# Optimization experiments

Hardware: AMD Instinct MI355X
Metric: run time of the kernel (lower is better)

Reference implementation:

```python
import jax, jax.numpy as jnp
import numpy as np

HIDDEN = 2048
REDUCTION = 4
DOWN = HIDDEN // REDUCTION  # 512
E = 16
K = 2
B, S = 4, 2048


def setup_inputs() -> dict:
    key = jax.random.key(0)
    k1, k2, k3, k4 = jax.random.split(key, 4)
    x = jax.random.normal(k1, (B, S, HIDDEN), dtype=jnp.float32)
    gate_w = jax.random.normal(k2, (E, HIDDEN), dtype=jnp.float32) * 0.02
    # xavier_uniform over (E, DOWN, HIDDEN): bound = sqrt(6/(DOWN+HIDDEN))
    bound = float(np.sqrt(6.0 / (DOWN + HIDDEN)))
    down_w = jax.random.uniform(k3, (E, DOWN, HIDDEN), dtype=jnp.float32,
                                minval=-bound, maxval=bound)
    down_b = jnp.zeros((E, DOWN), dtype=jnp.float32)
    ub = float(np.sqrt(1.0 / DOWN))
    up_w = jax.random.uniform(k4, (HIDDEN, DOWN), dtype=jnp.float32,
                              minval=-ub, maxval=ub)
    up_b = jnp.zeros((HIDDEN,), dtype=jnp.float32)
    return {"x": x, "gate_w": gate_w, "down_w": down_w, "down_b": down_b,
            "up_w": up_w, "up_b": up_b}


def reference(x, gate_w, down_w, down_b, up_w, up_b):
    Bb, Ss, D = x.shape
    N = Bb * Ss
    xf = x.reshape(N, D)
    # TopKGate: logits -> top-k -> softmax over the k logits -> scatter to full [N,E]
    logits = xf @ gate_w.T                       # [N, E]
    topv, topi = jax.lax.top_k(logits, K)        # [N, K]
    probs = jax.nn.softmax(topv, axis=-1)        # [N, K]
    gw = jnp.zeros_like(logits).at[jnp.arange(N)[:, None], topi].set(probs)  # [N, E]
    # Dense-equivalent of gather + per-token bmm + scatter-add combine:
    # final[n] = sum_e gw[n,e] * (down_w[e] @ x[n] + down_b[e])
    expert_out = jnp.einsum('nd,eod->neo', xf, down_w) + down_b[None]  # [N, E, DOWN]
    combined = jnp.einsum('ne,neo->no', gw, expert_out)                # [N, DOWN]
    h = jax.nn.gelu(combined, approximate=True)  # gelu_new (tanh approx)
    h = h.reshape(Bb, Ss, DOWN)
    out = h @ up_w.T + up_b                      # [B, S, HIDDEN]
    # load balancing loss: E * sum(sum(gw,0)/N * mean(gw,0)) * alpha
    loss = E * jnp.sum(jnp.sum(gw, axis=0) / N * jnp.mean(gw, axis=0)) * 0.1
    return out, loss
```

## Files before the change

kernel.cpp:

```cpp
#include <hip/hip_runtime.h>
#include <hip/hip_bf16.h>
#include <math.h>

#define NTOK   8192
#define HID    2048
#define DWN    512
#define NEXP   16
#define PADSLOT 18432
#define NSLOTBLK 144
#define DGRID_HALF (NSLOTBLK * (DWN / 128))

#define OFF_XB       0
#define OFF_DWB      33554432
#define OFF_H        33554432
#define OFF_UWB      67108864
#define OFF_TOK      69206016
#define OFF_SPOS     69279744
#define OFF_EIDX     69345280
#define OFF_PVAL     69410816
#define OFF_COUNTS   69476352
#define OFF_BASE     69476416
#define OFF_CURSOR   69476544
#define OFF_COLSUM   69476608
#define OFF_SEG      69476672
#define SEGHALF_SHORTS 9437184
#define SEGHALF_BYTES  18874368
#define WS_NEED1     (OFF_SEG + 1 * SEGHALF_BYTES)
#define WS_NEED2     (OFF_SEG + 2 * SEGHALF_BYTES)

typedef __attribute__((ext_vector_type(8))) __bf16 bf16x8;
typedef __attribute__((ext_vector_type(4))) float f32x4;

#define ASYNC16(gsrc, ldst) \
  __builtin_amdgcn_global_load_lds((const __attribute__((address_space(1))) unsigned int*)(gsrc), \
                                   (__attribute__((address_space(3))) unsigned int*)(ldst), 16, 0, 0)

#define VMWAIT_BAR(N) do { asm volatile("s_waitcnt vmcnt(" #N ")" ::: "memory"); \
                           __builtin_amdgcn_s_barrier(); } while (0)
#define NOSTMT ((void)0)

__device__ inline unsigned short f2bf(float f) {
  unsigned int u = __float_as_uint(f);
  unsigned int r = (u + 0x7FFFu + ((u >> 16) & 1u)) >> 16;
  return (unsigned short)r;
}
__device__ inline float bf2f(unsigned short s) {
  return __uint_as_float((unsigned int)s << 16);
}

__global__ __launch_bounds__(256) void cast8_kernel(const float* __restrict__ src,
                                                    unsigned short* __restrict__ dst)
{
  size_t i = ((size_t)blockIdx.x * 256 + threadIdx.x) * 8;
  float4 a = *(const float4*)(src + i);
  float4 b = *(const float4*)(src + i + 4);
  unsigned short o[8];
  o[0]=f2bf(a.x); o[1]=f2bf(a.y); o[2]=f2bf(a.z); o[3]=f2bf(a.w);
  o[4]=f2bf(b.x); o[5]=f2bf(b.y); o[6]=f2bf(b.z); o[7]=f2bf(b.w);
  *(uint4*)(dst + i) = *(const uint4*)o;
}

__global__ __launch_bounds__(256, 4) void gate_kernel(
    const float* __restrict__ x, const float* __restrict__ gw,
    int2* __restrict__ eidx, float2* __restrict__ pvals,
    unsigned short* __restrict__ xbw)
{
  __shared__ float gws[2][NEXP * 256];

  int lane = threadIdx.x & 63;
  int wave = threadIdx.x >> 6;
  int n0 = (blockIdx.x * 4 + wave) * 2;
  const float* xr0 = x + (size_t)n0 * HID;
  const float* xr1 = xr0 + HID;
  unsigned short* xw0 = xbw + (size_t)n0 * HID;
  unsigned short* xw1 = xw0 + HID;

  double acc0[NEXP], acc1[NEXP];
#pragma unroll
  for (int e = 0; e < NEXP; e++) { acc0[e] = 0.0; acc1[e] = 0.0; }

#pragma unroll
  for (int r = 0; r < 4; r++) {
    int e = r * 4 + wave;
    ASYNC16(gw + (size_t)e * HID + lane * 4, &gws[0][e * 256]);
  }
  __syncthreads();

  int cur = 0;
  for (int c = 0; c < HID / 256; c++) {
    int d0 = c * 256;
    if (c + 1 < HID / 256) {
#pragma unroll
      for (int r = 0; r < 4; r++) {
        int e = r * 4 + wave;
        ASYNC16(gw + (size_t)e * HID + d0 + 256 + lane * 4, &gws[cur ^ 1][e * 256]);
      }
    }
    int d = d0 + lane * 4;
    float4 xv0 = *(const float4*)(xr0 + d);
    float4 xv1 = *(const float4*)(xr1 + d);
    unsigned short o0[4] = {f2bf(xv0.x), f2bf(xv0.y), f2bf(xv0.z), f2bf(xv0.w)};
    unsigned short o1[4] = {f2bf(xv1.x), f2bf(xv1.y), f2bf(xv1.z), f2bf(xv1.w)};
    *(uint2*)(xw0 + d) = *(const uint2*)o0;
    *(uint2*)(xw1 + d) = *(const uint2*)o1;
    double x00 = (double)xv0.x, x01 = (double)xv0.y, x02 = (double)xv0.z, x03 = (double)xv0.w;
    double x10 = (double)xv1.x, x11 = (double)xv1.y, x12 = (double)xv1.z, x13 = (double)xv1.w;
    const float* gs = &gws[cur][lane * 4];
#pragma unroll
    for (int e = 0; e < NEXP; e++) {
      float4 g = *(const float4*)(gs + e * 256);
      double g0 = (double)g.x, g1 = (double)g.y, g2 = (double)g.z, g3 = (double)g.w;
      double s0 = acc0[e], s1 = acc1[e];
      s0 = fma(x00, g0, s0); s0 = fma(x01, g1, s0);
      s0 = fma(x02, g2, s0); s0 = fma(x03, g3, s0);
      s1 = fma(x10, g0, s1); s1 = fma(x11, g1, s1);
      s1 = fma(x12, g2, s1); s1 = fma(x13, g3, s1);
      acc0[e] = s0; acc1[e] = s1;
    }
    __syncthreads();
    cur ^= 1;
  }

#define RED(v) { v += __shfl_xor(v,32,64); v += __shfl_xor(v,16,64); v += __shfl_xor(v,8,64); \
                 v += __shfl_xor(v,4,64);  v += __shfl_xor(v,2,64);  v += __shfl_xor(v,1,64); }
#pragma unroll
  for (int e = 0; e < NEXP; e++) { RED(acc0[e]) RED(acc1[e]) }
#undef RED

#define TOPSEL(ACC, N) { \
    double v0 = -1e300, v1 = -1e300; int i0 = 0, i1 = 0; \
    _Pragma("unroll") \
    for (int e = 0; e < NEXP; e++) { \
      double v = ACC[e]; \
      if (v > v0) { v1 = v0; i1 = i0; v0 = v; i0 = e; } \
      else if (v > v1) { v1 = v; i1 = e; } \
    } \
    double ex = exp(v1 - v0); \
    double denom = 1.0 + ex; \
    eidx[N]  = make_int2(i0, i1); \
    pvals[N] = make_float2((float)(1.0 / denom), (float)(ex / denom)); \
  }
  if (lane == 0) TOPSEL(acc0, n0)
  if (lane == 1) TOPSEL(acc1, n0 + 1)
#undef TOPSEL
}

__global__ __launch_bounds__(256) void hist_kernel(
    const int2* __restrict__ eidx, const float2* __restrict__ pvals,
    int* __restrict__ counts, float* __restrict__ colsum)
{
  __shared__ int   cbin[NEXP];
  __shared__ float lbin[NEXP];
  if (threadIdx.x < NEXP) { cbin[threadIdx.x] = 0; lbin[threadIdx.x] = 0.f; }
  __syncthreads();
  int n = blockIdx.x * 256 + threadIdx.x;
  int2 e = eidx[n];
  float2 p = pvals[n];
  atomicAdd(&cbin[e.x], 1);  atomicAdd(&lbin[e.x], p.x);
  atomicAdd(&cbin[e.y], 1);  atomicAdd(&lbin[e.y], p.y);
  __syncthreads();
  if (threadIdx.x < NEXP) {
    atomicAdd(&counts[threadIdx.x], cbin[threadIdx.x]);
    atomicAdd(&colsum[threadIdx.x], lbin[threadIdx.x]);
  }
}

__global__ void scan_loss_kernel(const int* __restrict__ counts, int* __restrict__ base,
                                 const float* __restrict__ colsum, float* __restrict__ loss_out)
{
  if (threadIdx.x == 0 && blockIdx.x == 0) {
    int acc = 0;
    for (int e = 0; e < NEXP; e++) { base[e] = acc; acc += (counts[e] + 127) & ~127; }
    base[NEXP] = acc;
    double s = 0.0;
    for (int e = 0; e < NEXP; e++) { double c = (double)colsum[e]; s += c * c; }
    loss_out[0] = (float)(1.6 * s / ((double)NTOK * (double)NTOK));
  }
}

__global__ __launch_bounds__(256) void scatter_kernel(
    const int2* __restrict__ eidx, const int* __restrict__ base, int* __restrict__ cursor,
    int* __restrict__ tok, int2* __restrict__ spos)
{
  int n = blockIdx.x * 256 + threadIdx.x;
  int lane = threadIdx.x & 63;
  int2 e = eidx[n];
  int myE[2] = {e.x, e.y};
  int myPos[2];
#pragma unroll
  for (int s = 0; s < 2; s++) {
    int eq = myE[s];
#pragma unroll
    for (int q = 0; q < NEXP; q++) {
      unsigned long long m = __ballot(eq == q);
      if (eq == q) {
        int cnt = __popcll(m);
        int pre = __popcll(m & ((1ull << lane) - 1ull));
        int b = 0;
        if (pre == 0) b = atomicAdd(&cursor[q], cnt);
        int leader = __ffsll((long long)m) - 1;
        b = __shfl(b, leader, 64);
        int pos = base[q] + b + pre;
        tok[pos] = n;
        myPos[s] = pos;
      }
    }
  }
  spos[n] = make_int2(myPos[0], myPos[1]);
}

__global__ __launch_bounds__(256, 2) void down_mfma_kernel(
    const unsigned short* __restrict__ xb, const unsigned short* __restrict__ dwb,
    const int* __restrict__ base, const int* __restrict__ tok,
    unsigned short* __restrict__ seg, int kcount)
{
  __shared__ unsigned short smem[32768];

  int wg  = blockIdx.x;
  int cpx = gridDim.x >> 3;
  int logical = (wg & 7) * cpx + (wg >> 3);
  int kh      = logical / DGRID_HALF;
  int r       = logical % DGRID_HALF;
  int slot0   = (r >> 2) * 128;
  int out0    = (r & 3) * 128;

  if (slot0 >= base[NEXP]) return;
  int e = 0;
#pragma unroll
  for (int q = 1; q < NEXP; q++) if (base[q] <= slot0) e = q;
  int kbase = kh * kcount * 64;

  int tid = threadIdx.x;
  const int l = tid & 63, w = tid >> 6;
  const int wm = w & 1, wn = w >> 1;
  const int lm = l & 15, quad = l >> 4;

  const unsigned short* agp[4];
  const unsigned short* bgp[4];
#pragma unroll
  for (int i = 0; i < 4; i++) {
    int g = w * 4 + i;
    int rr = g * 8 + (l & 7);
    int kc = l >> 3;
    int t = tok[slot0 + rr];
    agp[i] = xb + (size_t)(t < 0 ? 0 : t) * HID + kbase + kc * 8;
    bgp[i] = dwb + ((size_t)e * DWN + out0 + rr) * HID + kbase + kc * 8;
  }

  int am_off[4], bn_off[4];
#pragma unroll
  for (int mi = 0; mi < 4; mi++) {
    int m = wm * 64 + mi * 16 + lm;
    am_off[mi] = (m >> 3) * 512 + (m & 7) * 8 + quad * 64;
    int nn = wn * 64 + mi * 16 + lm;
    bn_off[mi] = (nn >> 3) * 512 + (nn & 7) * 8 + quad * 64;
  }

  f32x4 acc[4][4] = {};
  bf16x8 a0[4], b0[4], a1[4], b1[4];

#define DSTAGE(BUF, T) do {                                                   \
    int k0_ = (T) * 64;                                                       \
    unsigned short* Ap_ = smem + (BUF) * 16384;                               \
    _Pragma("unroll") for (int i = 0; i < 4; i++) {                           \
      int g_ = w * 4 + i;                                                     \
      ASYNC16(agp[i] + k0_, &Ap_[g_ * 512]);                                  \
      ASYNC16(bgp[i] + k0_, &Ap_[8192 + g_ * 512]);                           \
    }                                                                         \
  } while (0)

#define DMFMA(AA, BB) do {                                                    \
    __builtin_amdgcn_s_setprio(1);                                            \
    _Pragma("unroll") for (int mi = 0; mi < 4; mi++)                          \
      _Pragma("unroll") for (int ni = 0; ni < 4; ni++)                        \
        acc[mi][ni] = __builtin_amdgcn_mfma_f32_16x16x32_bf16(AA[mi], BB[ni], acc[mi][ni], 0, 0, 0); \
    __builtin_amdgcn_s_setprio(0);                                            \
  } while (0)

  DSTAGE(0, 0);
  DSTAGE(1, 1);
  asm volatile("s_waitcnt vmcnt(8)" ::: "memory");
  __builtin_amdgcn_s_barrier();
#pragma unroll
  for (int mi = 0; mi < 4; mi++) {
    a0[mi] = *(const bf16x8*)&smem[am_off[mi]];
    b0[mi] = *(const bf16x8*)&smem[8192 + bn_off[mi]];
  }

  for (int it = 0; it < kcount; ++it) {
    int cur = it & 1;
    unsigned short* As = smem + cur * 16384;
    unsigned short* Bs = As + 8192;
#pragma unroll
    for (int mi = 0; mi < 4; mi++) {
      a1[mi] = *(const bf16x8*)&As[am_off[mi] + 256];
      b1[mi] = *(const bf16x8*)&Bs[bn_off[mi] + 256];
    }
    DMFMA(a0, b0);
    asm volatile("s_waitcnt lgkmcnt(0)" ::: "memory");
    __builtin_amdgcn_sched_barrier(0);
    __builtin_amdgcn_s_barrier();
    if (it + 2 < kcount) DSTAGE(cur, it + 2);
    if (it + 1 < kcount) {
      if (it + 2 < kcount) asm volatile("s_waitcnt vmcnt(8)" ::: "memory");
      else                 asm volatile("s_waitcnt vmcnt(0)" ::: "memory");
      __builtin_amdgcn_s_barrier();
      unsigned short* An = smem + (cur ^ 1) * 16384;
      unsigned short* Bn = An + 8192;
#pragma unroll
      for (int mi = 0; mi < 4; mi++) {
        a0[mi] = *(const bf16x8*)&An[am_off[mi]];
        b0[mi] = *(const bf16x8*)&Bn[bn_off[mi]];
      }
    }
    DMFMA(a1, b1);
  }
#undef DMFMA
#undef DSTAGE

  __syncthreads();
#pragma unroll
  for (int mi = 0; mi < 4; mi++)
#pragma unroll
    for (int reg = 0; reg < 4; reg++) {
      int m = wm * 64 + mi * 16 + quad * 4 + reg;
#pragma unroll
      for (int ni = 0; ni < 4; ni++) {
        int c = wn * 64 + ni * 16 + lm;
        smem[m * 136 + c] = f2bf(acc[mi][ni][reg]);
      }
    }
  __syncthreads();
#pragma unroll
  for (int it2 = 0; it2 < 8; it2++) {
    int chunk = it2 * 256 + tid;
    int row = chunk >> 4, off = (chunk & 15) * 8;
    uint4 v = *(const uint4*)&smem[row * 136 + off];
    *(uint4*)&seg[(size_t)kh * SEGHALF_SHORTS + (size_t)(slot0 + row) * 512 + out0 + off] = v;
  }
}

__global__ __launch_bounds__(256) void combine_gelu_kernel(
    const unsigned short* __restrict__ seg, const int2* __restrict__ spos,
    const float2* __restrict__ pv, const int2* __restrict__ eix,
    const float* __restrict__ db, unsigned short* __restrict__ h, int ksplit)
{
  int n = blockIdx.x * 4 + (threadIdx.x >> 6);
  int lane = threadIdx.x & 63;
  int c0 = lane * 8;
  int2 sp = spos[n];
  float2 p = pv[n];
  int2 e = eix[n];

  float d0[8] = {0,0,0,0,0,0,0,0}, d1[8] = {0,0,0,0,0,0,0,0};
  for (int hh = 0; hh < ksplit; hh++) {
    uint4 u0 = *(const uint4*)(seg + (size_t)hh * SEGHALF_SHORTS + (size_t)sp.x * 512 + c0);
    uint4 u1 = *(const uint4*)(seg + (size_t)hh * SEGHALF_SHORTS + (size_t)sp.y * 512 + c0);
    const unsigned short* s0 = (const unsigned short*)&u0;
    const unsigned short* s1 = (const unsigned short*)&u1;
#pragma unroll
    for (int j = 0; j < 8; j++) { d0[j] += bf2f(s0[j]); d1[j] += bf2f(s1[j]); }
  }
  float b0[8], b1[8];
  *(float4*)&b0[0] = *(const float4*)(db + e.x * DWN + c0);
  *(float4*)&b0[4] = *(const float4*)(db + e.x * DWN + c0 + 4);
  *(float4*)&b1[0] = *(const float4*)(db + e.y * DWN + c0);
  *(float4*)&b1[4] = *(const float4*)(db + e.y * DWN + c0 + 4);

  unsigned short o[8];
#pragma unroll
  for (int j = 0; j < 8; j++) {
    float xx = p.x * (d0[j] + b0[j]) + p.y * (d1[j] + b1[j]);
    float inner = 0.7978845608028654f * (xx + 0.044715f * xx * xx * xx);
    o[j] = f2bf(0.5f * xx * (1.0f + tanhf(inner)));
  }
  *(uint4*)(h + (size_t)n * DWN + c0) = *(const uint4*)o;
}

__global__ __launch_bounds__(512, 2) void up_mfma_kernel(
    const unsigned short* __restrict__ h, const unsigned short* __restrict__ uwb,
    const float* __restrict__ ub, float* __restrict__ out)
{
  __shared__ unsigned short smem[65536];

  int wg  = blockIdx.x;
  int cpx = gridDim.x >> 3;
  int logical = (wg & 7) * cpx + (wg >> 3);
  int row0 = (logical >> 3) * 256;
  int col0 = (logical & 7) * 256;

  int tid = threadIdx.x;
  const int l = tid & 63, w = tid >> 6;
  const int wm = w & 1, wn = w >> 1;
  const int lm = l & 15, quad = l >> 4;

  const unsigned short* agp[4];
  const unsigned short* bgp[4];
#pragma unroll
  for (int i = 0; i < 4; i++) {
    int g = w * 4 + i;
    int rr = g * 8 + (l & 7);
    int kc = l >> 3;
    agp[i] = h   + (size_t)(row0 + rr) * DWN + kc * 8;
    bgp[i] = uwb + (size_t)(col0 + rr) * DWN + kc * 8;
  }

  int am_off[8], bn_off[4];
#pragma unroll
  for (int mi = 0; mi < 8; mi++) {
    int m = wm * 128 + mi * 16 + lm;
    am_off[mi] = (m >> 3) * 512 + (m & 7) * 8 + quad * 64;
  }
#pragma unroll
  for (int ni = 0; ni < 4; ni++) {
    int nn = wn * 64 + ni * 16 + lm;
    bn_off[ni] = (nn >> 3) * 512 + (nn & 7) * 8 + quad * 64;
  }

  f32x4 acc[8][4] = {};

#define USTAGE(BUF, T) do {                                                   \
    int k0_ = (T) * 64;                                                       \
    unsigned short* Ap_ = smem + (BUF) * 32768;                               \
    _Pragma("unroll") for (int i = 0; i < 4; i++) {                           \
      int g_ = w * 4 + i;                                                     \
      ASYNC16(agp[i] + k0_, &Ap_[g_ * 512]);                                  \
      ASYNC16(bgp[i] + k0_, &Ap_[16384 + g_ * 512]);                          \
    }                                                                         \
  } while (0)

  USTAGE(0, 0);
  USTAGE(1, 1);
  asm volatile("s_waitcnt vmcnt(8)" ::: "memory");
  __builtin_amdgcn_s_barrier();

  int cur = 0;
#define UTILE(STAGE_STMT, WAIT_STMT) do {                                     \
    unsigned short* As = smem + cur * 32768;                                  \
    unsigned short* Bs = As + 16384;                                          \
    bf16x8 a0[8], b0[4], a1[8], b1[4];                                        \
    _Pragma("unroll") for (int mi = 0; mi < 8; mi++) a0[mi] = *(const bf16x8*)&As[am_off[mi]]; \
    _Pragma("unroll") for (int ni = 0; ni < 4; ni++) b0[ni] = *(const bf16x8*)&Bs[bn_off[ni]]; \
    __builtin_amdgcn_s_setprio(1);                                            \
    _Pragma("unroll") for (int mi = 0; mi < 8; mi++)                          \
      _Pragma("unroll") for (int ni = 0; ni < 4; ni++)                        \
        acc[mi][ni] = __builtin_amdgcn_mfma_f32_16x16x32_bf16(a0[mi], b0[ni], acc[mi][ni], 0, 0, 0); \
    __builtin_amdgcn_s_setprio(0);                                            \
    _Pragma("unroll") for (int mi = 0; mi < 8; mi++) a1[mi] = *(const bf16x8*)&As[am_off[mi] + 256]; \
    _Pragma("unroll") for (int ni = 0; ni < 4; ni++) b1[ni] = *(const bf16x8*)&Bs[bn_off[ni] + 256]; \
    asm volatile("s_waitcnt lgkmcnt(0)" ::: "memory");                        \
    __builtin_amdgcn_sched_barrier(0);                                        \
    __builtin_amdgcn_s_barrier();                                             \
    STAGE_STMT;                                                               \
    __builtin_amdgcn_s_setprio(1);                                            \
    _Pragma("unroll") for (int mi = 0; mi < 8; mi++)                          \
      _Pragma("unroll") for (int ni = 0; ni < 4; ni++)                        \
        acc[mi][ni] = __builtin_amdgcn_mfma_f32_16x16x32_bf16(a1[mi], b1[ni], acc[mi][ni], 0, 0, 0); \
    __builtin_amdgcn_s_setprio(0);                                            \
    WAIT_STMT;                                                                \
  } while (0)

  const int nt = DWN / 64;
  for (int it = 0; it < nt - 2; ++it) {
    UTILE(USTAGE(cur, it + 2), VMWAIT_BAR(8));
    cur ^= 1;
  }
  UTILE(NOSTMT, VMWAIT_BAR(0));
  cur ^= 1;
  UTILE(NOSTMT, NOSTMT);
#undef UTILE
#undef USTAGE

  float ubv[4];
#pragma unroll
  for (int ni = 0; ni < 4; ni++)
    ubv[ni] = ub[col0 + wn * 64 + ni * 16 + lm];
#pragma unroll
  for (int mi = 0; mi < 8; mi++) {
#pragma unroll
    for (int reg = 0; reg < 4; reg++) {
      int m = row0 + wm * 128 + mi * 16 + quad * 4 + reg;
      float* orow = out + (size_t)m * HID;
#pragma unroll
      for (int ni = 0; ni < 4; ni++) {
        int gc = col0 + wn * 64 + ni * 16 + lm;
        orow[gc] = acc[mi][ni][reg] + ubv[ni];
      }
    }
  }
}

extern "C" void kernel_launch(void* const* d_in, const int* in_sizes, int n_in,
                              void* d_out, int out_size, void* d_ws, size_t ws_size,
                              hipStream_t stream)
{
  const float* x  = (const float*)d_in[0];
  const float* gw = (const float*)d_in[1];
  const float* dw = (const float*)d_in[2];
  const float* db = (const float*)d_in[3];
  const float* uw = (const float*)d_in[4];
  const float* ub = (const float*)d_in[5];
  float* out = (float*)d_out;

  char* ws = (char*)d_ws;
  unsigned short* xb   = (unsigned short*)(ws + OFF_XB);
  unsigned short* dwb  = (unsigned short*)(ws + OFF_DWB);
  unsigned short* uwb  = (unsigned short*)(ws + OFF_UWB);
  unsigned short* h    = (unsigned short*)(ws + OFF_H);
  unsigned short* seg  = (unsigned short*)(ws + OFF_SEG);
  int*    tok    = (int*)(ws + OFF_TOK);
  int2*   spos   = (int2*)(ws + OFF_SPOS);
  int2*   eidx   = (int2*)(ws + OFF_EIDX);
  float2* pvals  = (float2*)(ws + OFF_PVAL);
  int*    counts = (int*)(ws + OFF_COUNTS);
  int*    base   = (int*)(ws + OFF_BASE);
  int*    cursor = (int*)(ws + OFF_CURSOR);
  float*  colsum = (float*)(ws + OFF_COLSUM);

  const int ksplit = (ws_size >= (size_t)WS_NEED2) ? 2 : 1;
  const int kcount = (HID / 64) / ksplit;

  hipMemsetAsync(tok, 0xFF, PADSLOT * sizeof(int), stream);
  hipMemsetAsync(counts, 0, 320, stream);

  cast8_kernel<<<(NEXP * DWN * HID) / 8 / 256, 256, 0, stream>>>(dw, dwb);
  cast8_kernel<<<(HID * DWN) / 8 / 256, 256, 0, stream>>>(uw, uwb);

  gate_kernel<<<NTOK / 8, 256, 0, stream>>>(x, gw, eidx, pvals, xb);
  hist_kernel<<<NTOK / 256, 256, 0, stream>>>(eidx, pvals, counts, colsum);
  scan_loss_kernel<<<1, 64, 0, stream>>>(counts, base, colsum, out + (size_t)NTOK * HID);
  scatter_kernel<<<NTOK / 256, 256, 0, stream>>>(eidx, base, cursor, tok, spos);

  down_mfma_kernel<<<DGRID_HALF * ksplit, 256, 0, stream>>>(xb, dwb, base, tok, seg, kcount);

  combine_gelu_kernel<<<NTOK / 4, 256, 0, stream>>>(seg, spos, pvals, eidx, db, h, ksplit);

  up_mfma_kernel<<<(NTOK / 256) * (HID / 256), 512, 0, stream>>>(h, uwb, ub, out);
}
```

Measured before the change: 372.6 us.

## Fuse histogram and scan into gate kernel and drop down-projection split-K

```diff
diff --git a/kernel.cpp b/kernel.cpp
--- a/kernel.cpp
+++ b/kernel.cpp
@@ -26,7 +26,6 @@
 #define SEGHALF_SHORTS 9437184
 #define SEGHALF_BYTES  18874368
 #define WS_NEED1     (OFF_SEG + 1 * SEGHALF_BYTES)
-#define WS_NEED2     (OFF_SEG + 2 * SEGHALF_BYTES)
 
 typedef __attribute__((ext_vector_type(8))) __bf16 bf16x8;
 typedef __attribute__((ext_vector_type(4))) float f32x4;
@@ -63,9 +62,14 @@
 __global__ __launch_bounds__(256, 4) void gate_kernel(
     const float* __restrict__ x, const float* __restrict__ gw,
     int2* __restrict__ eidx, float2* __restrict__ pvals,
-    unsigned short* __restrict__ xbw)
+    unsigned short* __restrict__ xbw,
+    int* __restrict__ counts, float* __restrict__ colsum,
+    int* __restrict__ base, float* __restrict__ loss_out)
 {
   __shared__ float gws[2][NEXP * 256];
+  __shared__ int   cbin[NEXP];
+  __shared__ float lbin[NEXP];
+  if (threadIdx.x < NEXP) { cbin[threadIdx.x] = 0; lbin[threadIdx.x] = 0.f; }
 
   int lane = threadIdx.x & 63;
   int wave = threadIdx.x >> 6;
@@ -137,44 +141,40 @@
     } \
     double ex = exp(v1 - v0); \
     double denom = 1.0 + ex; \
+    float p0 = (float)(1.0 / denom), p1 = (float)(ex / denom); \
     eidx[N]  = make_int2(i0, i1); \
-    pvals[N] = make_float2((float)(1.0 / denom), (float)(ex / denom)); \
+    pvals[N] = make_float2(p0, p1); \
+    atomicAdd(&cbin[i0], 1); atomicAdd(&lbin[i0], p0); \
+    atomicAdd(&cbin[i1], 1); atomicAdd(&lbin[i1], p1); \
   }
   if (lane == 0) TOPSEL(acc0, n0)
   if (lane == 1) TOPSEL(acc1, n0 + 1)
 #undef TOPSEL
-}
-
-__global__ __launch_bounds__(256) void hist_kernel(
-    const int2* __restrict__ eidx, const float2* __restrict__ pvals,
-    int* __restrict__ counts, float* __restrict__ colsum)
-{
-  __shared__ int   cbin[NEXP];
-  __shared__ float lbin[NEXP];
-  if (threadIdx.x < NEXP) { cbin[threadIdx.x] = 0; lbin[threadIdx.x] = 0.f; }
-  __syncthreads();
-  int n = blockIdx.x * 256 + threadIdx.x;
-  int2 e = eidx[n];
-  float2 p = pvals[n];
-  atomicAdd(&cbin[e.x], 1);  atomicAdd(&lbin[e.x], p.x);
-  atomicAdd(&cbin[e.y], 1);  atomicAdd(&lbin[e.y], p.y);
+
   __syncthreads();
   if (threadIdx.x < NEXP) {
-    atomicAdd(&counts[threadIdx.x], cbin[threadIdx.x]);
-    atomicAdd(&colsum[threadIdx.x], lbin[threadIdx.x]);
-  }
-}
-
-__global__ void scan_loss_kernel(const int* __restrict__ counts, int* __restrict__ base,
-                                 const float* __restrict__ colsum, float* __restrict__ loss_out)
-{
-  if (threadIdx.x == 0 && blockIdx.x == 0) {
-    int acc = 0;
-    for (int e = 0; e < NEXP; e++) { base[e] = acc; acc += (counts[e] + 127) & ~127; }
-    base[NEXP] = acc;
-    double s = 0.0;
-    for (int e = 0; e < NEXP; e++) { double c = (double)colsum[e]; s += c * c; }
-    loss_out[0] = (float)(1.6 * s / ((double)NTOK * (double)NTOK));
+    if (cbin[threadIdx.x]) {
+      atomicAdd(&counts[threadIdx.x], cbin[threadIdx.x]);
+      atomicAdd(&colsum[threadIdx.x], lbin[threadIdx.x]);
+    }
+  }
+  __threadfence();
+  __syncthreads();
+  if (threadIdx.x == 0) {
+    int t = atomicAdd(&base[20], 1);
+    if (t == (int)gridDim.x - 1) {
+      int acc = 0;
+      double s = 0.0;
+      for (int e = 0; e < NEXP; e++) {
+        int cc = atomicAdd(&counts[e], 0);
+        base[e] = acc; acc += (cc + 127) & ~127;
+        double cs = (double)atomicAdd(&colsum[e], 0.0f);
+        s += cs * cs;
+      }
+      base[NEXP] = acc;
+      loss_out[0] = (float)(1.6 * s / ((double)NTOK * (double)NTOK));
+      __threadfence();
+    }
   }
 }
 
@@ -219,8 +219,7 @@
   int wg  = blockIdx.x;
   int cpx = gridDim.x >> 3;
   int logical = (wg & 7) * cpx + (wg >> 3);
-  int kh      = logical / DGRID_HALF;
-  int r       = logical % DGRID_HALF;
+  int r       = logical;
   int slot0   = (r >> 2) * 128;
   int out0    = (r & 3) * 128;
 
@@ -228,7 +227,6 @@
   int e = 0;
 #pragma unroll
   for (int q = 1; q < NEXP; q++) if (base[q] <= slot0) e = q;
-  int kbase = kh * kcount * 64;
 
   int tid = threadIdx.x;
   const int l = tid & 63, w = tid >> 6;
@@ -243,8 +241,8 @@
     int rr = g * 8 + (l & 7);
     int kc = l >> 3;
     int t = tok[slot0 + rr];
-    agp[i] = xb + (size_t)(t < 0 ? 0 : t) * HID + kbase + kc * 8;
-    bgp[i] = dwb + ((size_t)e * DWN + out0 + rr) * HID + kbase + kc * 8;
+    agp[i] = xb + (size_t)(t < 0 ? 0 : t) * HID + kc * 8;
+    bgp[i] = dwb + ((size_t)e * DWN + out0 + rr) * HID + kc * 8;
   }
 
   int am_off[4], bn_off[4];
@@ -336,14 +334,14 @@
     int chunk = it2 * 256 + tid;
     int row = chunk >> 4, off = (chunk & 15) * 8;
     uint4 v = *(const uint4*)&smem[row * 136 + off];
-    *(uint4*)&seg[(size_t)kh * SEGHALF_SHORTS + (size_t)(slot0 + row) * 512 + out0 + off] = v;
+    *(uint4*)&seg[(size_t)(slot0 + row) * 512 + out0 + off] = v;
   }
 }
 
 __global__ __launch_bounds__(256) void combine_gelu_kernel(
     const unsigned short* __restrict__ seg, const int2* __restrict__ spos,
     const float2* __restrict__ pv, const int2* __restrict__ eix,
-    const float* __restrict__ db, unsigned short* __restrict__ h, int ksplit)
+    const float* __restrict__ db, unsigned short* __restrict__ h)
 {
   int n = blockIdx.x * 4 + (threadIdx.x >> 6);
   int lane = threadIdx.x & 63;
@@ -352,15 +350,11 @@
   float2 p = pv[n];
   int2 e = eix[n];
 
-  float d0[8] = {0,0,0,0,0,0,0,0}, d1[8] = {0,0,0,0,0,0,0,0};
-  for (int hh = 0; hh < ksplit; hh++) {
-    uint4 u0 = *(const uint4*)(seg + (size_t)hh * SEGHALF_SHORTS + (size_t)sp.x * 512 + c0);
-    uint4 u1 = *(const uint4*)(seg + (size_t)hh * SEGHALF_SHORTS + (size_t)sp.y * 512 + c0);
-    const unsigned short* s0 = (const unsigned short*)&u0;
-    const unsigned short* s1 = (const unsigned short*)&u1;
-#pragma unroll
-    for (int j = 0; j < 8; j++) { d0[j] += bf2f(s0[j]); d1[j] += bf2f(s1[j]); }
-  }
+  uint4 u0 = *(const uint4*)(seg + (size_t)sp.x * 512 + c0);
+  uint4 u1 = *(const uint4*)(seg + (size_t)sp.y * 512 + c0);
+  const unsigned short* s0 = (const unsigned short*)&u0;
+  const unsigned short* s1 = (const unsigned short*)&u1;
+
   float b0[8], b1[8];
   *(float4*)&b0[0] = *(const float4*)(db + e.x * DWN + c0);
   *(float4*)&b0[4] = *(const float4*)(db + e.x * DWN + c0 + 4);
@@ -370,7 +364,7 @@
   unsigned short o[8];
 #pragma unroll
   for (int j = 0; j < 8; j++) {
-    float xx = p.x * (d0[j] + b0[j]) + p.y * (d1[j] + b1[j]);
+    float xx = p.x * (bf2f(s0[j]) + b0[j]) + p.y * (bf2f(s1[j]) + b1[j]);
     float inner = 0.7978845608028654f * (xx + 0.044715f * xx * xx * xx);
     o[j] = f2bf(0.5f * xx * (1.0f + tanhf(inner)));
   }
@@ -517,8 +511,7 @@
   int*    cursor = (int*)(ws + OFF_CURSOR);
   float*  colsum = (float*)(ws + OFF_COLSUM);
 
-  const int ksplit = (ws_size >= (size_t)WS_NEED2) ? 2 : 1;
-  const int kcount = (HID / 64) / ksplit;
+  const int kcount = HID / 64;
 
   hipMemsetAsync(tok, 0xFF, PADSLOT * sizeof(int), stream);
   hipMemsetAsync(counts, 0, 320, stream);
@@ -526,14 +519,13 @@
   cast8_kernel<<<(NEXP * DWN * HID) / 8 / 256, 256, 0, stream>>>(dw, dwb);
   cast8_kernel<<<(HID * DWN) / 8 / 256, 256, 0, stream>>>(uw, uwb);
 
-  gate_kernel<<<NTOK / 8, 256, 0, stream>>>(x, gw, eidx, pvals, xb);
-  hist_kernel<<<NTOK / 256, 256, 0, stream>>>(eidx, pvals, counts, colsum);
-  scan_loss_kernel<<<1, 64, 0, stream>>>(counts, base, colsum, out + (size_t)NTOK * HID);
+  gate_kernel<<<NTOK / 8, 256, 0, stream>>>(x, gw, eidx, pvals, xb,
+                                            counts, colsum, base, out + (size_t)NTOK * HID);
   scatter_kernel<<<NTOK / 256, 256, 0, stream>>>(eidx, base, cursor, tok, spos);
 
-  down_mfma_kernel<<<DGRID_HALF * ksplit, 256, 0, stream>>>(xb, dwb, base, tok, seg, kcount);
-
-  combine_gelu_kernel<<<NTOK / 4, 256, 0, stream>>>(seg, spos, pvals, eidx, db, h, ksplit);
+  down_mfma_kernel<<<DGRID_HALF, 256, 0, stream>>>(xb, dwb, base, tok, seg, kcount);
+
+  combine_gelu_kernel<<<NTOK / 4, 256, 0, stream>>>(seg, spos, pvals, eidx, db, h);
 
   up_mfma_kernel<<<(NTOK / 256) * (HID / 256), 512, 0, stream>>>(h, uwb, ub, out);
 }
```

Result: slower. 476.8 us (+28.0%).

## Drop split-K in down-projection and merge weight cast launches

Applied to the files above, without the earlier changes.

```diff
diff --git a/kernel.cpp b/kernel.cpp
--- a/kernel.cpp
+++ b/kernel.cpp
@@ -9,6 +9,8 @@
 #define PADSLOT 18432
 #define NSLOTBLK 144
 #define DGRID_HALF (NSLOTBLK * (DWN / 128))
+#define CAST_DW_BLOCKS ((NEXP * DWN * HID) / 8 / 256)
+#define CAST_UW_BLOCKS ((HID * DWN) / 8 / 256)
 
 #define OFF_XB       0
 #define OFF_DWB      33554432
@@ -26,7 +28,6 @@
 #define SEGHALF_SHORTS 9437184
 #define SEGHALF_BYTES  18874368
 #define WS_NEED1     (OFF_SEG + 1 * SEGHALF_BYTES)
-#define WS_NEED2     (OFF_SEG + 2 * SEGHALF_BYTES)
 
 typedef __attribute__((ext_vector_type(8))) __bf16 bf16x8;
 typedef __attribute__((ext_vector_type(4))) float f32x4;
@@ -48,10 +49,21 @@
   return __uint_as_float((unsigned int)s << 16);
 }
 
-__global__ __launch_bounds__(256) void cast8_kernel(const float* __restrict__ src,
-                                                    unsigned short* __restrict__ dst)
-{
-  size_t i = ((size_t)blockIdx.x * 256 + threadIdx.x) * 8;
+__global__ __launch_bounds__(256) void cast_weights_kernel(const float* __restrict__ dw,
+                                                           unsigned short* __restrict__ dwb,
+                                                           const float* __restrict__ uw,
+                                                           unsigned short* __restrict__ uwb)
+{
+  const float* src;
+  unsigned short* dst;
+  size_t i;
+  if (blockIdx.x < CAST_DW_BLOCKS) {
+    src = dw; dst = dwb;
+    i = ((size_t)blockIdx.x * 256 + threadIdx.x) * 8;
+  } else {
+    src = uw; dst = uwb;
+    i = ((size_t)(blockIdx.x - CAST_DW_BLOCKS) * 256 + threadIdx.x) * 8;
+  }
   float4 a = *(const float4*)(src + i);
   float4 b = *(const float4*)(src + i + 4);
   unsigned short o[8];
@@ -219,8 +231,7 @@
   int wg  = blockIdx.x;
   int cpx = gridDim.x >> 3;
   int logical = (wg & 7) * cpx + (wg >> 3);
-  int kh      = logical / DGRID_HALF;
-  int r       = logical % DGRID_HALF;
+  int r       = logical;
   int slot0   = (r >> 2) * 128;
   int out0    = (r & 3) * 128;
 
@@ -228,7 +239,6 @@
   int e = 0;
 #pragma unroll
   for (int q = 1; q < NEXP; q++) if (base[q] <= slot0) e = q;
-  int kbase = kh * kcount * 64;
 
   int tid = threadIdx.x;
   const int l = tid & 63, w = tid >> 6;
@@ -243,8 +253,8 @@
     int rr = g * 8 + (l & 7);
     int kc = l >> 3;
     int t = tok[slot0 + rr];
-    agp[i] = xb + (size_t)(t < 0 ? 0 : t) * HID + kbase + kc * 8;
-    bgp[i] = dwb + ((size_t)e * DWN + out0 + rr) * HID + kbase + kc * 8;
+    agp[i] = xb + (size_t)(t < 0 ? 0 : t) * HID + kc * 8;
+    bgp[i] = dwb + ((size_t)e * DWN + out0 + rr) * HID + kc * 8;
   }
 
   int am_off[4], bn_off[4];
@@ -336,14 +346,14 @@
     int chunk = it2 * 256 + tid;
     int row = chunk >> 4, off = (chunk & 15) * 8;
     uint4 v = *(const uint4*)&smem[row * 136 + off];
-    *(uint4*)&seg[(size_t)kh * SEGHALF_SHORTS + (size_t)(slot0 + row) * 512 + out0 + off] = v;
+    *(uint4*)&seg[(size_t)(slot0 + row) * 512 + out0 + off] = v;
   }
 }
 
 __global__ __launch_bounds__(256) void combine_gelu_kernel(
     const unsigned short* __restrict__ seg, const int2* __restrict__ spos,
     const float2* __restrict__ pv, const int2* __restrict__ eix,
-    const float* __restrict__ db, unsigned short* __restrict__ h, int ksplit)
+    const float* __restrict__ db, unsigned short* __restrict__ h)
 {
   int n = blockIdx.x * 4 + (threadIdx.x >> 6);
   int lane = threadIdx.x & 63;
@@ -352,15 +362,11 @@
   float2 p = pv[n];
   int2 e = eix[n];
 
-  float d0[8] = {0,0,0,0,0,0,0,0}, d1[8] = {0,0,0,0,0,0,0,0};
-  for (int hh = 0; hh < ksplit; hh++) {
-    uint4 u0 = *(const uint4*)(seg + (size_t)hh * SEGHALF_SHORTS + (size_t)sp.x * 512 + c0);
-    uint4 u1 = *(const uint4*)(seg + (size_t)hh * SEGHALF_SHORTS + (size_t)sp.y * 512 + c0);
-    const unsigned short* s0 = (const unsigned short*)&u0;
-    const unsigned short* s1 = (const unsigned short*)&u1;
-#pragma unroll
-    for (int j = 0; j < 8; j++) { d0[j] += bf2f(s0[j]); d1[j] += bf2f(s1[j]); }
-  }
+  uint4 u0 = *(const uint4*)(seg + (size_t)sp.x * 512 + c0);
+  uint4 u1 = *(const uint4*)(seg + (size_t)sp.y * 512 + c0);
+  const unsigned short* s0 = (const unsigned short*)&u0;
+  const unsigned short* s1 = (const unsigned short*)&u1;
+
   float b0[8], b1[8];
   *(float4*)&b0[0] = *(const float4*)(db + e.x * DWN + c0);
   *(float4*)&b0[4] = *(const float4*)(db + e.x * DWN + c0 + 4);
@@ -370,7 +376,7 @@
   unsigned short o[8];
 #pragma unroll
   for (int j = 0; j < 8; j++) {
-    float xx = p.x * (d0[j] + b0[j]) + p.y * (d1[j] + b1[j]);
+    float xx = p.x * (bf2f(s0[j]) + b0[j]) + p.y * (bf2f(s1[j]) + b1[j]);
     float inner = 0.7978845608028654f * (xx + 0.044715f * xx * xx * xx);
     o[j] = f2bf(0.5f * xx * (1.0f + tanhf(inner)));
   }
@@ -517,23 +523,21 @@
   int*    cursor = (int*)(ws + OFF_CURSOR);
   float*  colsum = (float*)(ws + OFF_COLSUM);
 
-  const int ksplit = (ws_size >= (size_t)WS_NEED2) ? 2 : 1;
-  const int kcount = (HID / 64) / ksplit;
+  const int kcount = HID / 64;
 
   hipMemsetAsync(tok, 0xFF, PADSLOT * sizeof(int), stream);
   hipMemsetAsync(counts, 0, 320, stream);
 
-  cast8_kernel<<<(NEXP * DWN * HID) / 8 / 256, 256, 0, stream>>>(dw, dwb);
-  cast8_kernel<<<(HID * DWN) / 8 / 256, 256, 0, stream>>>(uw, uwb);
+  cast_weights_kernel<<<CAST_DW_BLOCKS + CAST_UW_BLOCKS, 256, 0, stream>>>(dw, dwb, uw, uwb);
 
   gate_kernel<<<NTOK / 8, 256, 0, stream>>>(x, gw, eidx, pvals, xb);
   hist_kernel<<<NTOK / 256, 256, 0, stream>>>(eidx, pvals, counts, colsum);
   scan_loss_kernel<<<1, 64, 0, stream>>>(counts, base, colsum, out + (size_t)NTOK * HID);
   scatter_kernel<<<NTOK / 256, 256, 0, stream>>>(eidx, base, cursor, tok, spos);
 
-  down_mfma_kernel<<<DGRID_HALF * ksplit, 256, 0, stream>>>(xb, dwb, base, tok, seg, kcount);
-
-  combine_gelu_kernel<<<NTOK / 4, 256, 0, stream>>>(seg, spos, pvals, eidx, db, h, ksplit);
+  down_mfma_kernel<<<DGRID_HALF, 256, 0, stream>>>(xb, dwb, base, tok, seg, kcount);
+
+  combine_gelu_kernel<<<NTOK / 4, 256, 0, stream>>>(seg, spos, pvals, eidx, db, h);
 
   up_mfma_kernel<<<(NTOK / 256) * (HID / 256), 512, 0, stream>>>(h, uwb, ub, out);
 }
```

Measured after the change: 379.2 us. No clear change (+1.8%).
